# Optimization experiments

Measured on AMD Instinct MI355X. Metric: run time of the kernel, lower is better.

## Reference

```python
import math
import jax, jax.numpy as jnp
import numpy as np

B, C, H, W, R, P = 4, 64, 128, 128, 5, 8


def circular_sample(x, r):
    """Bilinear ring sampling, grid_sample(align_corners=True, padding_mode='zeros') equivalent.
    x: [B,C,H,W]; returns [B,H,W,C,P]."""
    Bx, Cx, Hx, Wx = x.shape
    angles = jnp.linspace(0.0, 2.0 * math.pi, P + 1)[:-1]
    di = r * jnp.sin(angles)  # row offsets [P]
    dj = r * jnp.cos(angles)  # col offsets [P]
    yy = jnp.arange(Hx, dtype=x.dtype)[:, None, None] + di[None, None, :]  # [H,1,P]
    xx = jnp.arange(Wx, dtype=x.dtype)[None, :, None] + dj[None, None, :]  # [1,W,P]
    yy = jnp.broadcast_to(yy, (Hx, Wx, P))
    xx = jnp.broadcast_to(xx, (Hx, Wx, P))
    y0 = jnp.floor(yy); x0 = jnp.floor(xx)
    wy = yy - y0; wx = xx - x0
    y0i = y0.astype(jnp.int32); x0i = x0.astype(jnp.int32)

    def gather(yi, xi):
        valid = ((yi >= 0) & (yi < Hx) & (xi >= 0) & (xi < Wx)).astype(x.dtype)
        yc = jnp.clip(yi, 0, Hx - 1)
        xc = jnp.clip(xi, 0, Wx - 1)
        return x[:, :, yc, xc] * valid  # [B,C,H,W,P], zeros padding

    v00 = gather(y0i, x0i)
    v01 = gather(y0i, x0i + 1)
    v10 = gather(y0i + 1, x0i)
    v11 = gather(y0i + 1, x0i + 1)
    out = (v00 * (1 - wy) * (1 - wx) + v01 * (1 - wy) * wx
           + v10 * wy * (1 - wx) + v11 * wy * wx)
    return jnp.transpose(out, (0, 2, 3, 1, 4))  # [B,H,W,C,P] -> channel-major, point-minor


def setup_inputs() -> dict:
    key = jax.random.key(0)
    ks = jax.random.split(key, 3)
    x = jax.random.normal(ks[0], (B, C, H, W), dtype=jnp.float32)
    CP = C * P
    W1 = jax.random.normal(ks[1], (R, CP, 64), dtype=jnp.float32) / np.sqrt(CP)
    b1 = jnp.zeros((R, 64), dtype=jnp.float32)
    g1 = jnp.ones((R, 64), dtype=jnp.float32)
    bt1 = jnp.zeros((R, 64), dtype=jnp.float32)
    W2 = jax.random.normal(ks[2], (R, 64, C), dtype=jnp.float32) / 8.0
    b2 = jnp.zeros((R, C), dtype=jnp.float32)
    return {"x": x, "W1": W1, "b1": b1, "g1": g1, "bt1": bt1, "W2": W2, "b2": b2}


def reference(x, W1, b1, g1, bt1, W2, b2):
    Bx, Cx, Hx, Wx = x.shape
    acc = jnp.zeros((Bx, Hx * Wx, Cx), dtype=x.dtype)
    for r in range(R):  # small fixed radius loop, matches module structure
        feat = circular_sample(x, float(r)).reshape(Bx, Hx * Wx, Cx * P)
        h = feat @ W1[r] + b1[r]
        mu = jnp.mean(h, axis=-1, keepdims=True)
        var = jnp.mean((h - mu) ** 2, axis=-1, keepdims=True)
        h = (h - mu) / jnp.sqrt(var + 1e-5) * g1[r] + bt1[r]
        h = jax.nn.gelu(h, approximate=False)  # torch nn.GELU default = exact erf
        acc = acc + h @ W2[r] + b2[r]
    wts = jax.nn.sigmoid(acc).reshape(Bx, Hx, Wx, Cx).transpose(0, 3, 1, 2)
    return x * wts
```

## Files before the change

kernel.cpp:

```cpp
#include <hip/hip_runtime.h>
#include <math.h>

namespace {
constexpr int Hh = 128, Ww = 128;
constexpr int NDCAP = 48;
constexpr int UROW  = 56;

using short8 = __attribute__((ext_vector_type(8))) short;
using f32x4  = __attribute__((ext_vector_type(4))) float;

__device__ __forceinline__ unsigned short f2bf(float f) {
    union { float f; unsigned int u; } v; v.f = f;
    unsigned int u = v.u;
    unsigned int r = (u + 0x7FFFu + ((u >> 16) & 1u)) >> 16;
    return (unsigned short)r;
}

constexpr size_t XBF_OFF  = 0;
constexpr size_t W1P_OFF  = 8388608;
constexpr size_t W2P_OFF  = W1P_OFF + (size_t)484 * 4096;
constexpr size_t META_OFF = W2P_OFF + 40960;
constexpr size_t UOFF_OFF = META_OFF + 64;
constexpr size_t WVEC_OFF = UOFF_OFF + 1152;
constexpr size_t WS_NEED  = WVEC_OFF + 7680;
}

__global__ void rrf_table(int* __restrict__ meta, int* __restrict__ uoff,
                          float* __restrict__ wvec)
{
    __shared__ float grid[5][81][8];
    __shared__ unsigned char keep[5][81];
    __shared__ short dofs[5][81];
    __shared__ int nds[5];

    const int t = threadIdx.x;
    for (int i = t; i < 5 * 81 * 8; i += 512) ((float*)grid)[i] = 0.f;
    for (int i = t; i < 5 * UROW; i += 512) uoff[i] = 0;
    __syncthreads();

    if (t < 40) {
        int r = t >> 3, p = t & 7;
        float ang = (float)p * 0.78539818525314331f;
        float si = (float)sin((double)ang);
        float co = (float)cos((double)ang);
        float di = (float)r * si;
        float dj = (float)r * co;
        float y0f = floorf(di), x0f = floorf(dj);
        float wy = di - y0f, wx = dj - x0f;
        int y0 = (int)y0f, x0 = (int)x0f;
        float tw[4] = {(1.f - wy) * (1.f - wx), (1.f - wy) * wx,
                       wy * (1.f - wx), wy * wx};
        int ty[4] = {y0, y0, y0 + 1, y0 + 1};
        int tx[4] = {x0, x0 + 1, x0, x0 + 1};
        #pragma unroll
        for (int q = 0; q < 4; ++q) {
            if (fabsf(tw[q]) < 1e-6f) continue;
            grid[r][(ty[q] + 4) * 9 + (tx[q] + 4)][p] = tw[q];
        }
    }
    __syncthreads();

    if (t < 405) {
        int r = t / 81, ci = t - r * 81;
        float mx = 0.f;
        #pragma unroll
        for (int p = 0; p < 8; ++p) mx = fmaxf(mx, fabsf(grid[r][ci][p]));
        keep[r][ci] = (mx > 1e-6f) ? 1 : 0;
    }
    __syncthreads();

    if (t < 5) {
        int nd = 0;
        for (int ci = 0; ci < 81; ++ci) {
            dofs[t][ci] = (short)nd;
            nd += keep[t][ci];
        }
        nds[t] = nd;
    }
    __syncthreads();

    if (t < 405) {
        int r = t / 81, ci = t - r * 81;
        if (keep[r][ci]) {
            int d = dofs[r][ci];
            int iy = ci / 9, ix = ci - iy * 9;
            uoff[r * UROW + d] = (iy * 24 + (ix - 4)) * 80;
            #pragma unroll
            for (int p = 0; p < 8; ++p)
                wvec[(r * NDCAP + d) * 8 + p] = grid[r][ci][p];
        }
    }
    if (t == 0) {
        int base = 0;
        for (int r = 0; r < 5; ++r) {
            int nd  = nds[r];
            int ndp = (nd + 3) & ~3;
            meta[r]      = ndp;
            meta[5 + r]  = base;
            meta[11 + r] = nd;
            base += ndp;
        }
        meta[10] = base;
    }
}

__global__ void rrf_pack(const float* __restrict__ W1, const float* __restrict__ W2,
                         const int* __restrict__ meta, const float* __restrict__ wvec,
                         unsigned short* __restrict__ w1p, unsigned short* __restrict__ w2p)
{
    int bb = blockIdx.x;
    if (bb < 480) {
        int gid  = bb * 256 + threadIdx.x;
        int lane = gid & 63;
        int t    = (gid >> 6) & 3;
        int cc   = (gid >> 8) & 1;
        int rd   = gid >> 9;
        int r = rd / NDCAP, d = rd % NDCAP;
        if (r >= 5 || d >= meta[r]) return;
        int TOTP  = meta[10];
        int chunk = cc * TOTP + meta[5 + r] + d;
        unsigned short* dst = w1p + ((size_t)(chunk * 4 + t) * 64 + lane) * 8;
        if (d >= meta[11 + r]) {
            short8 z = {0,0,0,0,0,0,0,0};
            *(short8*)dst = z;
            return;
        }
        int n = t * 16 + (lane & 15);
        int cbase = cc * 32 + ((lane >> 4) << 3);
        const float* wv  = wvec + (r * NDCAP + d) * 8;
        const float* w1r = W1 + (size_t)r * 512 * 64;
        short8 o;
        #pragma unroll
        for (int j = 0; j < 8; ++j) {
            int c = cbase + j;
            float acc = 0.f;
            #pragma unroll
            for (int p = 0; p < 8; ++p)
                acc = fmaf(wv[p], w1r[(c * 8 + p) * 64 + n], acc);
            o[j] = (short)f2bf(acc);
        }
        *(short8*)dst = o;
    } else {
        int i = (bb - 480) * 256 + threadIdx.x;
        if (i < 20480) {
            int j    = i & 7;
            int lane = (i >> 3) & 63;
            int kc2  = (i >> 9) & 1;
            int t    = (i >> 10) & 3;
            int r    = i >> 12;
            int n = kc2 * 32 + ((lane >> 4) << 3) + j;
            int m = t * 16 + (lane & 15);
            w2p[i] = f2bf(W2[(r * 64 + n) * 64 + m]);
        }
    }
}

__global__ void rrf_xpose(const float* __restrict__ x, unsigned short* __restrict__ xbf)
{
    __shared__ float tl[64][65];
    int b   = blockIdx.x >> 8;
    int px0 = (blockIdx.x & 255) * 64;
    int tx = threadIdx.x & 63, ty = threadIdx.x >> 6;
    #pragma unroll
    for (int i = 0; i < 16; ++i) {
        int c = i * 4 + ty;
        tl[c][tx] = x[(((size_t)b * 64 + c) << 14) + px0 + tx];
    }
    __syncthreads();
    #pragma unroll
    for (int i = 0; i < 16; ++i) {
        int px = i * 4 + ty;
        xbf[(((size_t)b << 14) + px0 + px) * 64 + tx] = f2bf(tl[tx][px]);
    }
}

#define LDA6(K, CI) { const unsigned short* _q = ap + (size_t)(CI) * 2048 + tsel + (lane << 3); \
    A##K[0] = *(const short8*)(_q); A##K[1] = *(const short8*)(_q + 512); }

#define LDB6(K, U) {                                                                      \
    B##K[0] = *(const short8*)(tb + ((U) + lbq0));                                        \
    B##K[1] = *(const short8*)(tb + ((U) + lbq1)); }

#define MF6(K) {                                                                          \
    hv[0][0] = __builtin_amdgcn_mfma_f32_16x16x32_bf16(A##K[0], B##K[0], hv[0][0], 0, 0, 0); \
    hv[0][1] = __builtin_amdgcn_mfma_f32_16x16x32_bf16(A##K[0], B##K[1], hv[0][1], 0, 0, 0); \
    hv[1][0] = __builtin_amdgcn_mfma_f32_16x16x32_bf16(A##K[1], B##K[0], hv[1][0], 0, 0, 0); \
    hv[1][1] = __builtin_amdgcn_mfma_f32_16x16x32_bf16(A##K[1], B##K[1], hv[1][1], 0, 0, 0); }

__global__ __launch_bounds__(1024, 1)
void rrf_stencil6(const float* __restrict__ x, const unsigned short* __restrict__ xbf,
                  const unsigned short* __restrict__ w1p, const unsigned short* __restrict__ w2p,
                  const int* __restrict__ meta, const int* __restrict__ uoff,
                  const float* __restrict__ b1v, const float* __restrict__ g1v,
                  const float* __restrict__ btv, const float* __restrict__ b2v,
                  float* __restrict__ out)
{
    __shared__ __align__(16) unsigned short tile[2][23040];
    __shared__ __align__(16) unsigned short gbuf[16][16][72];
    __shared__ float wsum[2][8][2][16][2];
    __shared__ int uo_lds[5 * UROW];
    __shared__ int meta_lds[16];

    const int tid  = threadIdx.x;
    const int w    = tid >> 6;
    const int lane = tid & 63;
    const int col  = lane & 15;
    const int g    = lane >> 4;
    const int tp   = w & 1;
    const int pg   = w >> 1;
    const int tsel = tp * 1024;

    const int bid = blockIdx.x;
    const int b   = bid >> 6;
    const int r0  = ((bid >> 3) & 7) * 16;
    const int c0  = (bid & 7) * 16;

    const int lbq0 = ((2 * pg + 0) * 24 + col + 4) * 80 + g * 16;
    const int lbq1 = ((2 * pg + 1) * 24 + col + 4) * 80 + g * 16;

    if (tid < 5 * UROW) uo_lds[tid] = uoff[tid];
    if (tid < 16) meta_lds[tid] = meta[tid];

    if (tid < 576) {
        int s = tid;
        int trow = s / 24, tcol = s - trow * 24;
        int row = r0 - 4 + trow, cg = c0 - 4 + tcol;
        bool valid = ((unsigned)row < 128u) && ((unsigned)cg < 128u);
        unsigned short* d0 = &tile[0][s * 40];
        unsigned short* d1 = &tile[1][s * 40];
        if (valid) {
            const unsigned short* src =
                xbf + (((size_t)(b << 14)) + row * 128 + cg) * 64;
            #pragma unroll
            for (int k = 0; k < 4; ++k) {
                *(short8*)(d0 + k * 8) = *(const short8*)(src + k * 8);
                *(short8*)(d1 + k * 8) = *(const short8*)(src + 32 + k * 8);
            }
        } else {
            short8 z = {0, 0, 0, 0, 0, 0, 0, 0};
            #pragma unroll
            for (int k = 0; k < 4; ++k) {
                *(short8*)(d0 + k * 8) = z;
                *(short8*)(d1 + k * 8) = z;
            }
        }
    }
    __syncthreads();

    f32x4 acc2[4];
    #pragma unroll
    for (int t = 0; t < 4; ++t) acc2[t] = f32x4{0.f, 0.f, 0.f, 0.f};

    #pragma unroll 1
    for (int r = 0; r < 5; ++r) {
        f32x4 hv[2][2];
        #pragma unroll
        for (int t = 0; t < 2; ++t)
            #pragma unroll
            for (int q = 0; q < 2; ++q) hv[t][q] = f32x4{0.f, 0.f, 0.f, 0.f};

        const int ndp  = __builtin_amdgcn_readfirstlane(meta_lds[r]);
        const int base = __builtin_amdgcn_readfirstlane(meta_lds[5 + r]);
        const int TOTP = __builtin_amdgcn_readfirstlane(meta_lds[10]);
        const int* uo = uo_lds + r * UROW;

        #pragma unroll 1
        for (int cc = 0; cc < 2; ++cc) {
            const unsigned short* ap = w1p + (size_t)(cc * TOTP + base) * 2048;
            const char* tb = (const char*)(&tile[cc][0]);

            short8 A0[2], A1[2], A2[2], A3[2];
            short8 B0[2], B1[2], B2[2], B3[2];
            LDA6(0, 0) LDB6(0, uo[0])
            LDA6(1, 1) LDB6(1, uo[1])
            LDA6(2, 2) LDB6(2, uo[2])
            LDA6(3, 3) LDB6(3, uo[3])
            int u0 = uo[4], u1 = uo[5], u2 = uo[6], u3 = uo[7];
            #pragma unroll 1
            for (int d = 0; d < ndp; d += 4) {
                MF6(0) LDA6(0, d + 4) LDB6(0, u0)
                MF6(1) LDA6(1, d + 5) LDB6(1, u1)
                MF6(2) LDA6(2, d + 6) LDB6(2, u2)
                MF6(3) LDA6(3, d + 7) LDB6(3, u3)
                u0 = uo[d + 8];  u1 = uo[d + 9];
                u2 = uo[d + 10]; u3 = uo[d + 11];
            }
        }

        float b1r[2][4], g1r[2][4], btr[2][4];
        #pragma unroll
        for (int t = 0; t < 2; ++t)
            #pragma unroll
            for (int e = 0; e < 4; ++e) {
                int n = (2 * tp + t) * 16 + g * 4 + e;
                b1r[t][e] = b1v[r * 64 + n];
                g1r[t][e] = g1v[r * 64 + n];
                btr[t][e] = btv[r * 64 + n];
            }

        float hq[2][2][4];
        float sA[2], sB[2];
        #pragma unroll
        for (int q = 0; q < 2; ++q) {
            float s = 0.f, s2 = 0.f;
            #pragma unroll
            for (int t = 0; t < 2; ++t)
                #pragma unroll
                for (int e = 0; e < 4; ++e) {
                    float v = hv[t][q][e] + b1r[t][e];
                    hq[t][q][e] = v;
                    s += v;
                    s2 = fmaf(v, v, s2);
                }
            s  += __shfl_xor(s, 16);  s  += __shfl_xor(s, 32);
            s2 += __shfl_xor(s2, 16); s2 += __shfl_xor(s2, 32);
            sA[q] = s; sB[q] = s2;
        }
        if (g == 0) {
            #pragma unroll
            for (int q = 0; q < 2; ++q) {
                wsum[tp][pg][q][col][0] = sA[q];
                wsum[tp][pg][q][col][1] = sB[q];
            }
        }
        __syncthreads();

        #pragma unroll
        for (int q = 0; q < 2; ++q) {
            float so  = wsum[tp ^ 1][pg][q][col][0];
            float s2o = wsum[tp ^ 1][pg][q][col][1];
            const float mu = (sA[q] + so) * 0.015625f;
            const float ms = (sB[q] + s2o) * 0.015625f;
            const float rs = rsqrtf(ms - mu * mu + 1e-5f);
            const int row = 2 * pg + q;
            #pragma unroll
            for (int t = 0; t < 2; ++t) {
                float ge[4];
                #pragma unroll
                for (int e = 0; e < 4; ++e) {
                    float v = (hq[t][q][e] - mu) * rs * g1r[t][e] + btr[t][e];
                    ge[e] = 0.5f * v * (1.f + erff(v * 0.70710678118654752f));
                }
                int n0 = (2 * tp + t) * 16 + g * 4;
                *(unsigned int*)&gbuf[row][col][n0] =
                    (unsigned int)f2bf(ge[0]) | ((unsigned int)f2bf(ge[1]) << 16);
                *(unsigned int*)&gbuf[row][col][n0 + 2] =
                    (unsigned int)f2bf(ge[2]) | ((unsigned int)f2bf(ge[3]) << 16);
            }
        }
        __syncthreads();

        const unsigned short* a2base = w2p + (size_t)r * 4096 + (size_t)lane * 8;
        #pragma unroll
        for (int kc2 = 0; kc2 < 2; ++kc2) {
            short8 bf2 = *(const short8*)&gbuf[w][col][kc2 * 32 + g * 8];
            #pragma unroll
            for (int t = 0; t < 4; ++t) {
                short8 a2f = *(const short8*)(a2base + kc2 * 512 + t * 1024);
                acc2[t] = __builtin_amdgcn_mfma_f32_16x16x32_bf16(a2f, bf2, acc2[t], 0, 0, 0);
            }
        }
        if (r < 4) __syncthreads();
    }

    #pragma unroll
    for (int t = 0; t < 4; ++t) {
        #pragma unroll
        for (int e = 0; e < 4; ++e) {
            int m = t * 16 + g * 4 + e;
            float sb = b2v[m] + b2v[64 + m] + b2v[128 + m] + b2v[192 + m] + b2v[256 + m];
            float a = acc2[t][e] + sb;
            float wts = 1.f / (1.f + expf(-a));
            size_t off = (((size_t)b * 64 + m) << 14)
                       + (size_t)(r0 + w) * 128 + (c0 + col);
            out[off] = x[off] * wts;
        }
    }
}

__global__ void rrf_prepack(const float* __restrict__ W1, const float* __restrict__ W2,
                            unsigned short* __restrict__ w1p, unsigned short* __restrict__ w2p)
{
    int i = blockIdx.x * 256 + threadIdx.x;
    if (i < 163840) {
        int jq   = i & 7;
        int lane = (i >> 3) & 63;
        int kc   = (i >> 9) & 15;
        int t    = (i >> 13) & 3;
        int r    = i >> 15;
        int k = kc * 32 + ((lane >> 4) << 3) + jq;
        int n = t * 16 + (lane & 15);
        w1p[i] = f2bf(W1[(r * 512 + k) * 64 + n]);
    }
    if (i < 20480) {
        int jq   = i & 7;
        int lane = (i >> 3) & 63;
        int kc2  = (i >> 9) & 1;
        int t    = (i >> 10) & 3;
        int r    = i >> 12;
        int n = kc2 * 32 + ((lane >> 4) << 3) + jq;
        int m = t * 16 + (lane & 15);
        w2p[i] = f2bf(W2[(r * 64 + n) * 64 + m]);
    }
}

__global__ __launch_bounds__(256, 2)
void rrf_mfma(const float* __restrict__ x,
              const unsigned short* __restrict__ w1p, const unsigned short* __restrict__ w2p,
              const float* __restrict__ b1v, const float* __restrict__ g1v,
              const float* __restrict__ btv, const float* __restrict__ b2v,
              float* __restrict__ out)
{
    __shared__ unsigned short gbuf[4][16][72];

    const int tid  = threadIdx.x;
    const int w    = tid >> 6;
    const int lane = tid & 63;
    const int col  = lane & 15;
    const int g    = lane >> 4;

    const int bid  = blockIdx.x;
    const int b    = bid >> 8;
    const int rem  = bid & 255;
    const int irow = rem >> 1;
    const int j0   = (rem & 1) * 64;
    const int j    = j0 + w * 16 + col;

    const float fi = (float)irow;
    const float fj = (float)j;
    const float* xb = x + ((size_t)b << 20);

    f32x4 acc2[4] = {f32x4{0,0,0,0}, f32x4{0,0,0,0}, f32x4{0,0,0,0}, f32x4{0,0,0,0}};

    #pragma unroll 1
    for (int r = 0; r < 5; ++r) {
        int   o00[8], o01[8], o10[8], o11[8];
        float w00[8], w01[8], w10[8], w11[8];
        const float rf = (float)r;
        #pragma unroll
        for (int p = 0; p < 8; ++p) {
            float ang = (float)p * 0.78539818525314331f;
            float yy = fi + rf * sinf(ang);
            float xx = fj + rf * cosf(ang);
            float y0f = floorf(yy), x0f = floorf(xx);
            float wy = yy - y0f, wx = xx - x0f;
            int y0 = (int)y0f, x0i = (int)x0f;
            int y1 = y0 + 1,   x1  = x0i + 1;
            float m00 = (y0 >= 0 && y0 < Hh && x0i >= 0 && x0i < Ww) ? 1.f : 0.f;
            float m01 = (y0 >= 0 && y0 < Hh && x1  >= 0 && x1  < Ww) ? 1.f : 0.f;
            float m10 = (y1 >= 0 && y1 < Hh && x0i >= 0 && x0i < Ww) ? 1.f : 0.f;
            float m11 = (y1 >= 0 && y1 < Hh && x1  >= 0 && x1  < Ww) ? 1.f : 0.f;
            int y0c = y0 < 0 ? 0 : (y0 > Hh - 1 ? Hh - 1 : y0);
            int y1c = y1 < 0 ? 0 : (y1 > Hh - 1 ? Hh - 1 : y1);
            int x0c = x0i < 0 ? 0 : (x0i > Ww - 1 ? Ww - 1 : x0i);
            int x1c = x1 < 0 ? 0 : (x1 > Ww - 1 ? Ww - 1 : x1);
            w00[p] = (1.f - wy) * (1.f - wx) * m00;
            w01[p] = (1.f - wy) * wx * m01;
            w10[p] = wy * (1.f - wx) * m10;
            w11[p] = wy * wx * m11;
            o00[p] = (y0c * Ww + x0c) * 4;
            o01[p] = (y0c * Ww + x1c) * 4;
            o10[p] = (y1c * Ww + x0c) * 4;
            o11[p] = (y1c * Ww + x1c) * 4;
        }

        f32x4 hv[4] = {f32x4{0,0,0,0}, f32x4{0,0,0,0}, f32x4{0,0,0,0}, f32x4{0,0,0,0}};
        const unsigned short* abase0 = w1p + ((size_t)((r * 64) * 64 + lane)) * 8;
        #pragma unroll 2
        for (int kc = 0; kc < 16; ++kc) {
            const int c = (kc << 2) + g;
            const char* xp = (const char*)(xb + ((size_t)c << 14));
            short8 bfrag;
            #pragma unroll
            for (int p = 0; p < 8; ++p) {
                float v00 = *(const float*)(xp + o00[p]);
                float v01 = *(const float*)(xp + o01[p]);
                float v10 = *(const float*)(xp + o10[p]);
                float v11 = *(const float*)(xp + o11[p]);
                float v = w00[p] * v00;
                v = fmaf(w01[p], v01, v);
                v = fmaf(w10[p], v10, v);
                v = fmaf(w11[p], v11, v);
                bfrag[p] = (short)f2bf(v);
            }
            const unsigned short* ab = abase0 + (size_t)kc * 512;
            #pragma unroll
            for (int t = 0; t < 4; ++t) {
                short8 af = *(const short8*)(ab + (size_t)t * 8192);
                hv[t] = __builtin_amdgcn_mfma_f32_16x16x32_bf16(af, bfrag, hv[t], 0, 0, 0);
            }
        }

        const int nb = g << 2;
        float hq[4][4];
        float s = 0.f;
        #pragma unroll
        for (int t = 0; t < 4; ++t)
            #pragma unroll
            for (int q = 0; q < 4; ++q) {
                float hvq = hv[t][q] + b1v[r * 64 + t * 16 + nb + q];
                hq[t][q] = hvq;
                s += hvq;
            }
        s += __shfl_xor(s, 16);
        s += __shfl_xor(s, 32);
        const float mu = s * 0.015625f;
        float s2 = 0.f;
        #pragma unroll
        for (int t = 0; t < 4; ++t)
            #pragma unroll
            for (int q = 0; q < 4; ++q) {
                float d = hq[t][q] - mu;
                s2 = fmaf(d, d, s2);
            }
        s2 += __shfl_xor(s2, 16);
        s2 += __shfl_xor(s2, 32);
        const float rs = rsqrtf(s2 * 0.015625f + 1e-5f);

        #pragma unroll
        for (int t = 0; t < 4; ++t)
            #pragma unroll
            for (int q = 0; q < 4; ++q) {
                int n = t * 16 + nb + q;
                float v = (hq[t][q] - mu) * rs * g1v[r * 64 + n] + btv[r * 64 + n];
                hq[t][q] = 0.5f * v * (1.f + erff(v * 0.70710678118654752f));
            }
        #pragma unroll
        for (int t = 0; t < 4; ++t) {
            #pragma unroll
            for (int q2 = 0; q2 < 4; q2 += 2) {
                unsigned int u = (unsigned int)f2bf(hq[t][q2])
                               | ((unsigned int)f2bf(hq[t][q2 + 1]) << 16);
                *(unsigned int*)&gbuf[w][col][t * 16 + nb + q2] = u;
            }
        }

        const unsigned short* a2base = w2p + ((size_t)((r * 8) * 64 + lane)) * 8;
        #pragma unroll
        for (int kc2 = 0; kc2 < 2; ++kc2) {
            short8 bf2 = *(const short8*)&gbuf[w][col][kc2 * 32 + g * 8];
            const unsigned short* a2 = a2base + (size_t)kc2 * 512;
            #pragma unroll
            for (int t = 0; t < 4; ++t) {
                short8 a2f = *(const short8*)(a2 + (size_t)t * 1024);
                acc2[t] = __builtin_amdgcn_mfma_f32_16x16x32_bf16(a2f, bf2, acc2[t], 0, 0, 0);
            }
        }
    }

    #pragma unroll
    for (int t = 0; t < 4; ++t) {
        #pragma unroll
        for (int q = 0; q < 4; ++q) {
            int m = t * 16 + (g << 2) + q;
            float sb = b2v[m] + b2v[64 + m] + b2v[128 + m] + b2v[192 + m] + b2v[256 + m];
            float a = acc2[t][q] + sb;
            float wts = 1.f / (1.f + expf(-a));
            size_t off = (((size_t)b * 64 + m) << 14) + ((size_t)irow << 7) + j;
            out[off] = x[off] * wts;
        }
    }
}

extern "C" void kernel_launch(void* const* d_in, const int* in_sizes, int n_in,
                              void* d_out, int out_size, void* d_ws, size_t ws_size,
                              hipStream_t stream)
{
    const float* x  = (const float*)d_in[0];
    const float* W1 = (const float*)d_in[1];
    const float* b1 = (const float*)d_in[2];
    const float* g1 = (const float*)d_in[3];
    const float* bt = (const float*)d_in[4];
    const float* W2 = (const float*)d_in[5];
    const float* b2 = (const float*)d_in[6];
    float* outp = (float*)d_out;
    char* ws = (char*)d_ws;

    if (ws_size >= WS_NEED) {
        unsigned short* xbf = (unsigned short*)(ws + XBF_OFF);
        unsigned short* w1p = (unsigned short*)(ws + W1P_OFF);
        unsigned short* w2p = (unsigned short*)(ws + W2P_OFF);
        int*   meta  = (int*)(ws + META_OFF);
        int*   uoffp = (int*)(ws + UOFF_OFF);
        float* wvec  = (float*)(ws + WVEC_OFF);

        rrf_xpose<<<dim3(1024), dim3(256), 0, stream>>>(x, xbf);
        rrf_table<<<dim3(1), dim3(512), 0, stream>>>(meta, uoffp, wvec);
        rrf_pack<<<dim3(564), dim3(256), 0, stream>>>(W1, W2, meta, wvec, w1p, w2p);
        rrf_stencil6<<<dim3(256), dim3(1024), 0, stream>>>(x, xbf, w1p, w2p, meta, uoffp,
                                                           b1, g1, bt, b2, outp);
    } else {
        unsigned short* w1p = (unsigned short*)d_ws;
        unsigned short* w2p = w1p + 163840;
        rrf_prepack<<<dim3(640), dim3(256), 0, stream>>>(W1, W2, w1p, w2p);
        rrf_mfma<<<dim3(1024), dim3(256), 0, stream>>>(x, w1p, w2p, b1, g1, bt, b2, outp);
    }
}
```

Measured before the change: 97.39 us.

## Split K across wave pairs with dword-interleaved LDS tile and exchange reductions

Restructures the main stencil GEMM so each wave owns one input-channel half (kc) and computes 4 pixel rows by 32 hidden units. A fragments are loaded once per stencil tap, halving global weight loads per MFMA. The LDS tile is re-laid out as interleaved dwords so B fragments come from 16 conflict-free 4-byte reads, and partial sums are exchanged between wave pairs through LDS in bf16. The GELU output is redistributed with shuffles instead of a gbuf round trip, which also drops the trailing barrier. The cost is more LDS reads per tap, higher register pressure, and extra bf16 rounding of the split-K partial sums.

Result: slower. 151.9 us (+55.9%).

```diff
diff --git a/kernel.cpp b/kernel.cpp
--- a/kernel.cpp
+++ b/kernel.cpp
@@ -15,6 +15,14 @@
     unsigned int r = (u + 0x7FFFu + ((u >> 16) & 1u)) >> 16;
     return (unsigned short)r;
 }
+__device__ __forceinline__ float bflo(unsigned int u) {
+    union { unsigned int u; float f; } v; v.u = u << 16; return v.f;
+}
+__device__ __forceinline__ float bfhi(unsigned int u) {
+    union { unsigned int u; float f; } v; v.u = u & 0xffff0000u; return v.f;
+}
+
+union U8 { unsigned int d[4]; short8 s; };
 
 constexpr size_t XBF_OFF  = 0;
 constexpr size_t W1P_OFF  = 8388608;
@@ -84,7 +92,7 @@
         if (keep[r][ci]) {
             int d = dofs[r][ci];
             int iy = ci / 9, ix = ci - iy * 9;
-            uoff[r * UROW + d] = (iy * 24 + (ix - 4)) * 80;
+            uoff[r * UROW + d] = (iy * 24 + (ix - 4)) * 4;
             #pragma unroll
             for (int p = 0; p < 8; ++p)
                 wvec[(r * NDCAP + d) * 8 + p] = grid[r][ci][p];
@@ -174,30 +182,35 @@
     }
 }
 
-#define LDA6(K, CI) { const unsigned short* _q = ap + (size_t)(CI) * 2048 + tsel + (lane << 3); \
-    A##K[0] = *(const short8*)(_q); A##K[1] = *(const short8*)(_q + 512); }
-
-#define LDB6(K, U) {                                                                      \
-    B##K[0] = *(const short8*)(tb + ((U) + lbq0));                                        \
-    B##K[1] = *(const short8*)(tb + ((U) + lbq1)); }
-
-#define MF6(K) {                                                                          \
-    hv[0][0] = __builtin_amdgcn_mfma_f32_16x16x32_bf16(A##K[0], B##K[0], hv[0][0], 0, 0, 0); \
-    hv[0][1] = __builtin_amdgcn_mfma_f32_16x16x32_bf16(A##K[0], B##K[1], hv[0][1], 0, 0, 0); \
-    hv[1][0] = __builtin_amdgcn_mfma_f32_16x16x32_bf16(A##K[1], B##K[0], hv[1][0], 0, 0, 0); \
-    hv[1][1] = __builtin_amdgcn_mfma_f32_16x16x32_bf16(A##K[1], B##K[1], hv[1][1], 0, 0, 0); }
+#define LDBANK7(AA, BB, D, UU) {                                                          \
+    const unsigned short* _p = ap + (size_t)(D) * 2048;                                   \
+    AA[0] = *(const short8*)(_p); AA[1] = *(const short8*)(_p + 512);                     \
+    const char* _tc = tb_lane + (UU);                                                     \
+    _Pragma("unroll")                                                                     \
+    for (int _q = 0; _q < 4; ++_q)                                                        \
+        _Pragma("unroll")                                                                 \
+        for (int _j = 0; _j < 4; ++_j)                                                    \
+            BB[_q].d[_j] = *(const unsigned int*)(_tc + _j * 9472 + _q * 96); }
+
+#define MFBANK7(AA, BB) {                                                                 \
+    _Pragma("unroll")                                                                     \
+    for (int _t = 0; _t < 2; ++_t)                                                        \
+        _Pragma("unroll")                                                                 \
+        for (int _q = 0; _q < 4; ++_q)                                                    \
+            hv[_t][_q] = __builtin_amdgcn_mfma_f32_16x16x32_bf16(AA[_t], BB[_q].s,        \
+                                                                 hv[_t][_q], 0, 0, 0); }
 
 __global__ __launch_bounds__(1024, 1)
-void rrf_stencil6(const float* __restrict__ x, const unsigned short* __restrict__ xbf,
+void rrf_stencil7(const float* __restrict__ x, const unsigned short* __restrict__ xbf,
                   const unsigned short* __restrict__ w1p, const unsigned short* __restrict__ w2p,
                   const int* __restrict__ meta, const int* __restrict__ uoff,
                   const float* __restrict__ b1v, const float* __restrict__ g1v,
                   const float* __restrict__ btv, const float* __restrict__ b2v,
                   float* __restrict__ out)
 {
-    __shared__ __align__(16) unsigned short tile[2][23040];
-    __shared__ __align__(16) unsigned short gbuf[16][16][72];
-    __shared__ float wsum[2][8][2][16][2];
+    __shared__ __align__(16) unsigned int tile_u32[18944];
+    __shared__ __align__(16) unsigned char exch[49152];
+    __shared__ float wsum[2][16][16][2];
     __shared__ int uo_lds[5 * UROW];
     __shared__ int meta_lds[16];
 
@@ -206,85 +219,112 @@
     const int lane = tid & 63;
     const int col  = lane & 15;
     const int g    = lane >> 4;
-    const int tp   = w & 1;
-    const int pg   = w >> 1;
-    const int tsel = tp * 1024;
+    const int kc   = w & 1;
+    const int np   = (w >> 1) & 1;
+    const int pg   = w >> 2;
 
     const int bid = blockIdx.x;
     const int b   = bid >> 6;
     const int r0  = ((bid >> 3) & 7) * 16;
     const int c0  = (bid & 7) * 16;
 
-    const int lbq0 = ((2 * pg + 0) * 24 + col + 4) * 80 + g * 16;
-    const int lbq1 = ((2 * pg + 1) * 24 + col + 4) * 80 + g * 16;
-
     if (tid < 5 * UROW) uo_lds[tid] = uoff[tid];
-    if (tid < 16) meta_lds[tid] = meta[tid];
+    if (tid >= 5 * UROW && tid < 5 * UROW + 16) meta_lds[tid - 5 * UROW] = meta[tid - 5 * UROW];
 
     if (tid < 576) {
         int s = tid;
         int trow = s / 24, tcol = s - trow * 24;
         int row = r0 - 4 + trow, cg = c0 - 4 + tcol;
         bool valid = ((unsigned)row < 128u) && ((unsigned)cg < 128u);
-        unsigned short* d0 = &tile[0][s * 40];
-        unsigned short* d1 = &tile[1][s * 40];
         if (valid) {
             const unsigned short* src =
                 xbf + (((size_t)(b << 14)) + row * 128 + cg) * 64;
             #pragma unroll
-            for (int k = 0; k < 4; ++k) {
-                *(short8*)(d0 + k * 8) = *(const short8*)(src + k * 8);
-                *(short8*)(d1 + k * 8) = *(const short8*)(src + 32 + k * 8);
-            }
+            for (int h = 0; h < 2; ++h)
+                #pragma unroll
+                for (int k = 0; k < 4; ++k) {
+                    U8 u; u.s = *(const short8*)(src + h * 32 + k * 8);
+                    #pragma unroll
+                    for (int j = 0; j < 4; ++j)
+                        tile_u32[h * 9472 + (j * 4 + k) * 592 + s] = u.d[j];
+                }
         } else {
-            short8 z = {0, 0, 0, 0, 0, 0, 0, 0};
-            #pragma unroll
-            for (int k = 0; k < 4; ++k) {
-                *(short8*)(d0 + k * 8) = z;
-                *(short8*)(d1 + k * 8) = z;
-            }
+            #pragma unroll
+            for (int h = 0; h < 2; ++h)
+                #pragma unroll
+                for (int k = 0; k < 4; ++k)
+                    #pragma unroll
+                    for (int j = 0; j < 4; ++j)
+                        tile_u32[h * 9472 + (j * 4 + k) * 592 + s] = 0u;
         }
     }
     __syncthreads();
+
+    const int P004 = ((4 * pg) * 24 + col + 4) * 4;
+    const char* tb_lane = (const char*)tile_u32 + kc * 37888 + g * 2368 + P004;
 
     f32x4 acc2[4];
     #pragma unroll
     for (int t = 0; t < 4; ++t) acc2[t] = f32x4{0.f, 0.f, 0.f, 0.f};
 
+    const int src0 = 32 * (g & 1) + col;
+    const int src1 = src0 + 16;
+    const bool ghi = (g >> 1) != 0;
+    const int R16 = 4 * pg + 2 * kc;
+    unsigned char* exw = exch + w * 3072 + lane * 48;
+
     #pragma unroll 1
     for (int r = 0; r < 5; ++r) {
-        f32x4 hv[2][2];
+        f32x4 hv[2][4];
         #pragma unroll
         for (int t = 0; t < 2; ++t)
             #pragma unroll
-            for (int q = 0; q < 2; ++q) hv[t][q] = f32x4{0.f, 0.f, 0.f, 0.f};
+            for (int q = 0; q < 4; ++q) hv[t][q] = f32x4{0.f, 0.f, 0.f, 0.f};
 
         const int ndp  = __builtin_amdgcn_readfirstlane(meta_lds[r]);
         const int base = __builtin_amdgcn_readfirstlane(meta_lds[5 + r]);
         const int TOTP = __builtin_amdgcn_readfirstlane(meta_lds[10]);
         const int* uo = uo_lds + r * UROW;
-
+        const unsigned short* ap = w1p + (size_t)(kc * TOTP + base) * 2048
+                                 + np * 1024 + lane * 8;
+
+        short8 A0[2], A1[2];
+        U8 B0[4], B1[4];
+        LDBANK7(A0, B0, 0, uo[0])
+        LDBANK7(A1, B1, 1, uo[1])
         #pragma unroll 1
-        for (int cc = 0; cc < 2; ++cc) {
-            const unsigned short* ap = w1p + (size_t)(cc * TOTP + base) * 2048;
-            const char* tb = (const char*)(&tile[cc][0]);
-
-            short8 A0[2], A1[2], A2[2], A3[2];
-            short8 B0[2], B1[2], B2[2], B3[2];
-            LDA6(0, 0) LDB6(0, uo[0])
-            LDA6(1, 1) LDB6(1, uo[1])
-            LDA6(2, 2) LDB6(2, uo[2])
-            LDA6(3, 3) LDB6(3, uo[3])
-            int u0 = uo[4], u1 = uo[5], u2 = uo[6], u3 = uo[7];
-            #pragma unroll 1
-            for (int d = 0; d < ndp; d += 4) {
-                MF6(0) LDA6(0, d + 4) LDB6(0, u0)
-                MF6(1) LDA6(1, d + 5) LDB6(1, u1)
-                MF6(2) LDA6(2, d + 6) LDB6(2, u2)
-                MF6(3) LDA6(3, d + 7) LDB6(3, u3)
-                u0 = uo[d + 8];  u1 = uo[d + 9];
-                u2 = uo[d + 10]; u3 = uo[d + 11];
-            }
+        for (int d = 0; d < ndp; d += 2) {
+            int u2 = uo[d + 2], u3 = uo[d + 3];
+            MFBANK7(A0, B0)
+            LDBANK7(A0, B0, d + 2, u2)
+            __builtin_amdgcn_sched_barrier(0);
+            MFBANK7(A1, B1)
+            LDBANK7(A1, B1, d + 3, u3)
+            __builtin_amdgcn_sched_barrier(0);
+        }
+
+        {
+            unsigned int pk1[8];
+            #pragma unroll
+            for (int t = 0; t < 2; ++t) {
+                f32x4 gv0 = kc ? hv[t][0] : hv[t][2];
+                f32x4 gv1 = kc ? hv[t][1] : hv[t][3];
+                pk1[t * 4 + 0] = (unsigned int)f2bf(gv0[0]) | ((unsigned int)f2bf(gv0[1]) << 16);
+                pk1[t * 4 + 1] = (unsigned int)f2bf(gv0[2]) | ((unsigned int)f2bf(gv0[3]) << 16);
+                pk1[t * 4 + 2] = (unsigned int)f2bf(gv1[0]) | ((unsigned int)f2bf(gv1[1]) << 16);
+                pk1[t * 4 + 3] = (unsigned int)f2bf(gv1[2]) | ((unsigned int)f2bf(gv1[3]) << 16);
+            }
+            *(uint4*)(exw)      = make_uint4(pk1[0], pk1[1], pk1[2], pk1[3]);
+            *(uint4*)(exw + 16) = make_uint4(pk1[4], pk1[5], pk1[6], pk1[7]);
+        }
+        __syncthreads();
+        unsigned int rr[8];
+        {
+            const unsigned char* exr = exch + (w ^ 1) * 3072 + lane * 48;
+            uint4 ra = *(const uint4*)(exr);
+            uint4 rb = *(const uint4*)(exr + 16);
+            rr[0] = ra.x; rr[1] = ra.y; rr[2] = ra.z; rr[3] = ra.w;
+            rr[4] = rb.x; rr[5] = rb.y; rr[6] = rb.z; rr[7] = rb.w;
         }
 
         float b1r[2][4], g1r[2][4], btr[2][4];
@@ -292,77 +332,118 @@
         for (int t = 0; t < 2; ++t)
             #pragma unroll
             for (int e = 0; e < 4; ++e) {
-                int n = (2 * tp + t) * 16 + g * 4 + e;
+                int n = np * 32 + t * 16 + g * 4 + e;
                 b1r[t][e] = b1v[r * 64 + n];
                 g1r[t][e] = g1v[r * 64 + n];
                 btr[t][e] = btv[r * 64 + n];
             }
-
         float hq[2][2][4];
+        #pragma unroll
+        for (int t = 0; t < 2; ++t) {
+            f32x4 k0 = kc ? hv[t][2] : hv[t][0];
+            f32x4 k1 = kc ? hv[t][3] : hv[t][1];
+            unsigned int a0 = rr[t * 4 + 0], a1 = rr[t * 4 + 1];
+            unsigned int a2 = rr[t * 4 + 2], a3 = rr[t * 4 + 3];
+            hq[0][t][0] = k0[0] + bflo(a0) + b1r[t][0];
+            hq[0][t][1] = k0[1] + bfhi(a0) + b1r[t][1];
+            hq[0][t][2] = k0[2] + bflo(a1) + b1r[t][2];
+            hq[0][t][3] = k0[3] + bfhi(a1) + b1r[t][3];
+            hq[1][t][0] = k1[0] + bflo(a2) + b1r[t][0];
+            hq[1][t][1] = k1[1] + bfhi(a2) + b1r[t][1];
+            hq[1][t][2] = k1[2] + bflo(a3) + b1r[t][2];
+            hq[1][t][3] = k1[3] + bfhi(a3) + b1r[t][3];
+        }
         float sA[2], sB[2];
         #pragma unroll
-        for (int q = 0; q < 2; ++q) {
+        for (int i = 0; i < 2; ++i) {
             float s = 0.f, s2 = 0.f;
             #pragma unroll
             for (int t = 0; t < 2; ++t)
                 #pragma unroll
                 for (int e = 0; e < 4; ++e) {
-                    float v = hv[t][q][e] + b1r[t][e];
-                    hq[t][q][e] = v;
+                    float v = hq[i][t][e];
                     s += v;
                     s2 = fmaf(v, v, s2);
                 }
             s  += __shfl_xor(s, 16);  s  += __shfl_xor(s, 32);
             s2 += __shfl_xor(s2, 16); s2 += __shfl_xor(s2, 32);
-            sA[q] = s; sB[q] = s2;
+            sA[i] = s; sB[i] = s2;
         }
         if (g == 0) {
             #pragma unroll
-            for (int q = 0; q < 2; ++q) {
-                wsum[tp][pg][q][col][0] = sA[q];
-                wsum[tp][pg][q][col][1] = sB[q];
+            for (int i = 0; i < 2; ++i) {
+                wsum[np][R16 + i][col][0] = sA[i];
+                wsum[np][R16 + i][col][1] = sB[i];
             }
         }
         __syncthreads();
 
-        #pragma unroll
-        for (int q = 0; q < 2; ++q) {
-            float so  = wsum[tp ^ 1][pg][q][col][0];
-            float s2o = wsum[tp ^ 1][pg][q][col][1];
-            const float mu = (sA[q] + so) * 0.015625f;
-            const float ms = (sB[q] + s2o) * 0.015625f;
+        unsigned int pk[2][2][2];
+        #pragma unroll
+        for (int i = 0; i < 2; ++i) {
+            float so  = wsum[np ^ 1][R16 + i][col][0];
+            float s2o = wsum[np ^ 1][R16 + i][col][1];
+            const float mu = (sA[i] + so) * 0.015625f;
+            const float ms = (sB[i] + s2o) * 0.015625f;
             const float rs = rsqrtf(ms - mu * mu + 1e-5f);
-            const int row = 2 * pg + q;
             #pragma unroll
             for (int t = 0; t < 2; ++t) {
                 float ge[4];
                 #pragma unroll
                 for (int e = 0; e < 4; ++e) {
-                    float v = (hq[t][q][e] - mu) * rs * g1r[t][e] + btr[t][e];
+                    float v = (hq[i][t][e] - mu) * rs * g1r[t][e] + btr[t][e];
                     ge[e] = 0.5f * v * (1.f + erff(v * 0.70710678118654752f));
                 }
-                int n0 = (2 * tp + t) * 16 + g * 4;
-                *(unsigned int*)&gbuf[row][col][n0] =
-                    (unsigned int)f2bf(ge[0]) | ((unsigned int)f2bf(ge[1]) << 16);
-                *(unsigned int*)&gbuf[row][col][n0 + 2] =
-                    (unsigned int)f2bf(ge[2]) | ((unsigned int)f2bf(ge[3]) << 16);
-            }
+                pk[i][t][0] = (unsigned int)f2bf(ge[0]) | ((unsigned int)f2bf(ge[1]) << 16);
+                pk[i][t][1] = (unsigned int)f2bf(ge[2]) | ((unsigned int)f2bf(ge[3]) << 16);
+            }
+        }
+        {
+            unsigned int gv0 = np ? pk[0][0][0] : pk[1][0][0];
+            unsigned int gv1 = np ? pk[0][0][1] : pk[1][0][1];
+            unsigned int gv2 = np ? pk[0][1][0] : pk[1][1][0];
+            unsigned int gv3 = np ? pk[0][1][1] : pk[1][1][1];
+            *(uint4*)(exw + 32) = make_uint4(gv0, gv1, gv2, gv3);
         }
         __syncthreads();
+        unsigned int pkf[2][4];
+        {
+            uint4 gp = *(const uint4*)(exch + (w ^ 2) * 3072 + lane * 48 + 32);
+            unsigned int kp0 = np ? pk[1][0][0] : pk[0][0][0];
+            unsigned int kp1 = np ? pk[1][0][1] : pk[0][0][1];
+            unsigned int kp2 = np ? pk[1][1][0] : pk[0][1][0];
+            unsigned int kp3 = np ? pk[1][1][1] : pk[0][1][1];
+            pkf[0][0] = np ? gp.x : kp0;  pkf[1][0] = np ? kp0 : gp.x;
+            pkf[0][1] = np ? gp.y : kp1;  pkf[1][1] = np ? kp1 : gp.y;
+            pkf[0][2] = np ? gp.z : kp2;  pkf[1][2] = np ? kp2 : gp.z;
+            pkf[0][3] = np ? gp.w : kp3;  pkf[1][3] = np ? kp3 : gp.w;
+        }
 
         const unsigned short* a2base = w2p + (size_t)r * 4096 + (size_t)lane * 8;
         #pragma unroll
         for (int kc2 = 0; kc2 < 2; ++kc2) {
-            short8 bf2 = *(const short8*)&gbuf[w][col][kc2 * 32 + g * 8];
+            unsigned int d0a = (unsigned int)__shfl((int)pkf[kc2][0], src0);
+            unsigned int d0b = (unsigned int)__shfl((int)pkf[kc2][2], src0);
+            unsigned int d1a = (unsigned int)__shfl((int)pkf[kc2][1], src0);
+            unsigned int d1b = (unsigned int)__shfl((int)pkf[kc2][3], src0);
+            unsigned int d2a = (unsigned int)__shfl((int)pkf[kc2][0], src1);
+            unsigned int d2b = (unsigned int)__shfl((int)pkf[kc2][2], src1);
+            unsigned int d3a = (unsigned int)__shfl((int)pkf[kc2][1], src1);
+            unsigned int d3b = (unsigned int)__shfl((int)pkf[kc2][3], src1);
+            U8 u;
+            u.d[0] = ghi ? d0b : d0a;
+            u.d[1] = ghi ? d1b : d1a;
+            u.d[2] = ghi ? d2b : d2a;
+            u.d[3] = ghi ? d3b : d3a;
             #pragma unroll
             for (int t = 0; t < 4; ++t) {
                 short8 a2f = *(const short8*)(a2base + kc2 * 512 + t * 1024);
-                acc2[t] = __builtin_amdgcn_mfma_f32_16x16x32_bf16(a2f, bf2, acc2[t], 0, 0, 0);
-            }
-        }
-        if (r < 4) __syncthreads();
-    }
-
+                acc2[t] = __builtin_amdgcn_mfma_f32_16x16x32_bf16(a2f, u.s, acc2[t], 0, 0, 0);
+            }
+        }
+    }
+
+    const int Rg = r0 + 4 * pg + 2 * kc + np;
     #pragma unroll
     for (int t = 0; t < 4; ++t) {
         #pragma unroll
@@ -371,8 +452,7 @@
             float sb = b2v[m] + b2v[64 + m] + b2v[128 + m] + b2v[192 + m] + b2v[256 + m];
             float a = acc2[t][e] + sb;
             float wts = 1.f / (1.f + expf(-a));
-            size_t off = (((size_t)b * 64 + m) << 14)
-                       + (size_t)(r0 + w) * 128 + (c0 + col);
+            size_t off = (((size_t)b * 64 + m) << 14) + (size_t)Rg * 128 + (c0 + col);
             out[off] = x[off] * wts;
         }
     }
@@ -587,7 +667,7 @@
         rrf_xpose<<<dim3(1024), dim3(256), 0, stream>>>(x, xbf);
         rrf_table<<<dim3(1), dim3(512), 0, stream>>>(meta, uoffp, wvec);
         rrf_pack<<<dim3(564), dim3(256), 0, stream>>>(W1, W2, meta, wvec, w1p, w2p);
-        rrf_stencil6<<<dim3(256), dim3(1024), 0, stream>>>(x, xbf, w1p, w2p, meta, uoffp,
+        rrf_stencil7<<<dim3(256), dim3(1024), 0, stream>>>(x, xbf, w1p, w2p, meta, uoffp,
                                                            b1, g1, bt, b2, outp);
     } else {
         unsigned short* w1p = (unsigned short*)d_ws;
```

## Halve stencil tile to 8 rows with 512-thread blocks and shuffle-based GELU exchange

Applied to the files above, without the earlier changes.

The main stencil kernel now processes 8x16 pixel tiles with 512-thread blocks instead of 16x16 tiles with 1024 threads, doubling the grid and allowing several blocks per CU. The LDS gbuf staging of the GELU output is replaced by a small uint4 exchange between paired waves plus lane shuffles that build the second-GEMM B operand. The trailing per-radius barrier is dropped. This is meant to raise occupancy and cut LDS traffic and barriers. In exchange, each block loads more halo relative to its output tile, and the shuffles add VALU work.

New measurement: 89.76 us. 1.09x faster.

```diff
diff --git a/kernel.cpp b/kernel.cpp
--- a/kernel.cpp
+++ b/kernel.cpp
@@ -15,6 +15,8 @@
     unsigned int r = (u + 0x7FFFu + ((u >> 16) & 1u)) >> 16;
     return (unsigned short)r;
 }
+
+union U8 { unsigned int d[4]; short8 s; };
 
 constexpr size_t XBF_OFF  = 0;
 constexpr size_t W1P_OFF  = 8388608;
@@ -187,17 +189,17 @@
     hv[1][0] = __builtin_amdgcn_mfma_f32_16x16x32_bf16(A##K[1], B##K[0], hv[1][0], 0, 0, 0); \
     hv[1][1] = __builtin_amdgcn_mfma_f32_16x16x32_bf16(A##K[1], B##K[1], hv[1][1], 0, 0, 0); }
 
-__global__ __launch_bounds__(1024, 1)
-void rrf_stencil6(const float* __restrict__ x, const unsigned short* __restrict__ xbf,
+__global__ __launch_bounds__(512, 4)
+void rrf_stencil8(const float* __restrict__ x, const unsigned short* __restrict__ xbf,
                   const unsigned short* __restrict__ w1p, const unsigned short* __restrict__ w2p,
                   const int* __restrict__ meta, const int* __restrict__ uoff,
                   const float* __restrict__ b1v, const float* __restrict__ g1v,
                   const float* __restrict__ btv, const float* __restrict__ b2v,
                   float* __restrict__ out)
 {
-    __shared__ __align__(16) unsigned short tile[2][23040];
-    __shared__ __align__(16) unsigned short gbuf[16][16][72];
-    __shared__ float wsum[2][8][2][16][2];
+    __shared__ __align__(16) unsigned short tile[2][15360];
+    __shared__ __align__(16) uint4 exch[512];
+    __shared__ float wsum[2][8][16][2];
     __shared__ int uo_lds[5 * UROW];
     __shared__ int meta_lds[16];
 
@@ -211,17 +213,17 @@
     const int tsel = tp * 1024;
 
     const int bid = blockIdx.x;
-    const int b   = bid >> 6;
-    const int r0  = ((bid >> 3) & 7) * 16;
+    const int b   = bid >> 7;
+    const int r0  = ((bid >> 3) & 15) * 8;
     const int c0  = (bid & 7) * 16;
 
     const int lbq0 = ((2 * pg + 0) * 24 + col + 4) * 80 + g * 16;
     const int lbq1 = ((2 * pg + 1) * 24 + col + 4) * 80 + g * 16;
 
     if (tid < 5 * UROW) uo_lds[tid] = uoff[tid];
-    if (tid < 16) meta_lds[tid] = meta[tid];
-
-    if (tid < 576) {
+    if (tid >= 5 * UROW && tid < 5 * UROW + 16) meta_lds[tid - 5 * UROW] = meta[tid - 5 * UROW];
+
+    if (tid < 384) {
         int s = tid;
         int trow = s / 24, tcol = s - trow * 24;
         int row = r0 - 4 + trow, cg = c0 - 4 + tcol;
@@ -250,6 +252,11 @@
     f32x4 acc2[4];
     #pragma unroll
     for (int t = 0; t < 4; ++t) acc2[t] = f32x4{0.f, 0.f, 0.f, 0.f};
+
+    const int src0 = 32 * (g & 1) + col;
+    const int src1 = src0 + 16;
+    const bool ghi = (g >> 1) != 0;
+    const int R8 = 2 * pg;
 
     #pragma unroll 1
     for (int r = 0; r < 5; ++r) {
@@ -319,20 +326,20 @@
         if (g == 0) {
             #pragma unroll
             for (int q = 0; q < 2; ++q) {
-                wsum[tp][pg][q][col][0] = sA[q];
-                wsum[tp][pg][q][col][1] = sB[q];
+                wsum[tp][R8 + q][col][0] = sA[q];
+                wsum[tp][R8 + q][col][1] = sB[q];
             }
         }
         __syncthreads();
 
+        unsigned int pk[2][2][2];
         #pragma unroll
         for (int q = 0; q < 2; ++q) {
-            float so  = wsum[tp ^ 1][pg][q][col][0];
-            float s2o = wsum[tp ^ 1][pg][q][col][1];
+            float so  = wsum[tp ^ 1][R8 + q][col][0];
+            float s2o = wsum[tp ^ 1][R8 + q][col][1];
             const float mu = (sA[q] + so) * 0.015625f;
             const float ms = (sB[q] + s2o) * 0.015625f;
             const float rs = rsqrtf(ms - mu * mu + 1e-5f);
-            const int row = 2 * pg + q;
             #pragma unroll
             for (int t = 0; t < 2; ++t) {
                 float ge[4];
@@ -341,28 +348,51 @@
                     float v = (hq[t][q][e] - mu) * rs * g1r[t][e] + btr[t][e];
                     ge[e] = 0.5f * v * (1.f + erff(v * 0.70710678118654752f));
                 }
-                int n0 = (2 * tp + t) * 16 + g * 4;
-                *(unsigned int*)&gbuf[row][col][n0] =
-                    (unsigned int)f2bf(ge[0]) | ((unsigned int)f2bf(ge[1]) << 16);
-                *(unsigned int*)&gbuf[row][col][n0 + 2] =
-                    (unsigned int)f2bf(ge[2]) | ((unsigned int)f2bf(ge[3]) << 16);
-            }
+                pk[q][t][0] = (unsigned int)f2bf(ge[0]) | ((unsigned int)f2bf(ge[1]) << 16);
+                pk[q][t][1] = (unsigned int)f2bf(ge[2]) | ((unsigned int)f2bf(ge[3]) << 16);
+            }
+        }
+
+        {
+            int ig = tp ^ 1;
+            exch[tid] = make_uint4(pk[ig][0][0], pk[ig][0][1], pk[ig][1][0], pk[ig][1][1]);
         }
         __syncthreads();
+        unsigned int pkf[4][2];
+        {
+            uint4 po = exch[(w ^ 1) * 64 + lane];
+            pkf[2 * tp + 0][0] = pk[tp][0][0];  pkf[2 * tp + 0][1] = pk[tp][0][1];
+            pkf[2 * tp + 1][0] = pk[tp][1][0];  pkf[2 * tp + 1][1] = pk[tp][1][1];
+            int ot = 2 * (tp ^ 1);
+            pkf[ot + 0][0] = po.x;  pkf[ot + 0][1] = po.y;
+            pkf[ot + 1][0] = po.z;  pkf[ot + 1][1] = po.w;
+        }
 
         const unsigned short* a2base = w2p + (size_t)r * 4096 + (size_t)lane * 8;
         #pragma unroll
         for (int kc2 = 0; kc2 < 2; ++kc2) {
-            short8 bf2 = *(const short8*)&gbuf[w][col][kc2 * 32 + g * 8];
+            unsigned int d0a = (unsigned int)__shfl((int)pkf[kc2 * 2][0],     src0);
+            unsigned int d0b = (unsigned int)__shfl((int)pkf[kc2 * 2 + 1][0], src0);
+            unsigned int d1a = (unsigned int)__shfl((int)pkf[kc2 * 2][1],     src0);
+            unsigned int d1b = (unsigned int)__shfl((int)pkf[kc2 * 2 + 1][1], src0);
+            unsigned int d2a = (unsigned int)__shfl((int)pkf[kc2 * 2][0],     src1);
+            unsigned int d2b = (unsigned int)__shfl((int)pkf[kc2 * 2 + 1][0], src1);
+            unsigned int d3a = (unsigned int)__shfl((int)pkf[kc2 * 2][1],     src1);
+            unsigned int d3b = (unsigned int)__shfl((int)pkf[kc2 * 2 + 1][1], src1);
+            U8 u;
+            u.d[0] = ghi ? d0b : d0a;
+            u.d[1] = ghi ? d1b : d1a;
+            u.d[2] = ghi ? d2b : d2a;
+            u.d[3] = ghi ? d3b : d3a;
             #pragma unroll
             for (int t = 0; t < 4; ++t) {
                 short8 a2f = *(const short8*)(a2base + kc2 * 512 + t * 1024);
-                acc2[t] = __builtin_amdgcn_mfma_f32_16x16x32_bf16(a2f, bf2, acc2[t], 0, 0, 0);
-            }
-        }
-        if (r < 4) __syncthreads();
-    }
-
+                acc2[t] = __builtin_amdgcn_mfma_f32_16x16x32_bf16(a2f, u.s, acc2[t], 0, 0, 0);
+            }
+        }
+    }
+
+    const int Rg = r0 + 2 * pg + tp;
     #pragma unroll
     for (int t = 0; t < 4; ++t) {
         #pragma unroll
@@ -371,8 +401,7 @@
             float sb = b2v[m] + b2v[64 + m] + b2v[128 + m] + b2v[192 + m] + b2v[256 + m];
             float a = acc2[t][e] + sb;
             float wts = 1.f / (1.f + expf(-a));
-            size_t off = (((size_t)b * 64 + m) << 14)
-                       + (size_t)(r0 + w) * 128 + (c0 + col);
+            size_t off = (((size_t)b * 64 + m) << 14) + (size_t)Rg * 128 + (c0 + col);
             out[off] = x[off] * wts;
         }
     }
@@ -587,8 +616,8 @@
         rrf_xpose<<<dim3(1024), dim3(256), 0, stream>>>(x, xbf);
         rrf_table<<<dim3(1), dim3(512), 0, stream>>>(meta, uoffp, wvec);
         rrf_pack<<<dim3(564), dim3(256), 0, stream>>>(W1, W2, meta, wvec, w1p, w2p);
-        rrf_stencil6<<<dim3(256), dim3(1024), 0, stream>>>(x, xbf, w1p, w2p, meta, uoffp,
-                                                           b1, g1, bt, b2, outp);
+        rrf_stencil8<<<dim3(512), dim3(512), 0, stream>>>(x, xbf, w1p, w2p, meta, uoffp,
+                                                          b1, g1, bt, b2, outp);
     } else {
         unsigned short* w1p = (unsigned short*)d_ws;
         unsigned short* w2p = w1p + 163840;
```
